# Kernel optimization log

Measured on AMD Instinct MI355X. Metric: run time of the kernel, lower is better.

The kernel has to match this reference:

```python
import jax, jax.numpy as jnp
import numpy as np

IN_F, OUT_F = 1024, 1024
NUM, K = 5, 3            # pykan defaults: num grid intervals, spline degree
X_RANGE = 1.0
LN_EPS = 1e-5
BATCH = 4096


def _make_grid():
    # pykan: linspace over [-R, R] with num+1 points, extended by k points of
    # uniform spacing h on each side -> (in_dim, num + 2k + 1)
    g = np.linspace(-X_RANGE, X_RANGE, NUM + 1)
    h = (g[-1] - g[0]) / NUM
    ext = np.concatenate([g[0] - h * np.arange(K, 0, -1), g, g[-1] + h * np.arange(1, K + 1)])
    grid = np.broadcast_to(ext, (IN_F, NUM + 2 * K + 1)).copy()
    return jnp.asarray(grid, dtype=jnp.float32)


def setup_inputs() -> dict:
    key = jax.random.key(0)
    ks = jax.random.split(key, 4)
    x = jax.random.uniform(ks[0], (BATCH, IN_F), jnp.float32, -1.0, 1.0)
    coef = jax.random.normal(ks[1], (IN_F, OUT_F, NUM + K), jnp.float32) * 0.1
    scale_base = jax.random.normal(ks[2], (IN_F, OUT_F), jnp.float32) / jnp.sqrt(jnp.float32(IN_F))
    scale_sp = jnp.ones((IN_F, OUT_F), jnp.float32)
    gamma = jnp.ones((OUT_F,), jnp.float32)   # LayerNorm weight
    beta = jnp.zeros((OUT_F,), jnp.float32)   # LayerNorm bias
    return {"x": x, "coef": coef, "scale_base": scale_base, "scale_sp": scale_sp,
            "gamma": gamma, "beta": beta, "grid": _make_grid()}


def _b_splines(x, grid, k):
    # Cox-de Boor recursion, exactly as pykan B_batch (uniform grid -> no NaNs).
    # x: (B, in), grid: (in, G) -> basis (B, in, NUM + k)
    xe = x[:, :, None]
    g = grid[None, :, :]
    B = ((xe >= g[:, :, :-1]) & (xe < g[:, :, 1:])).astype(x.dtype)
    for p in range(1, k + 1):
        B = ((xe - g[:, :, :-(p + 1)]) / (g[:, :, p:-1] - g[:, :, :-(p + 1)]) * B[:, :, :-1]
             + (g[:, :, p + 1:] - xe) / (g[:, :, p + 1:] - g[:, :, 1:-p]) * B[:, :, 1:])
    return B


def reference(x, coef, scale_base, scale_sp, gamma, beta, grid):
    basis = _b_splines(x, grid, K)                        # (B, in, NUM+K)
    spline = jnp.einsum('bik,iok->bio', basis, coef)      # (B, in, out)
    base = jax.nn.silu(x)                                 # (B, in)  pykan base_fun
    y = scale_base[None, :, :] * base[:, :, None] + scale_sp[None, :, :] * spline
    y = jnp.sum(y, axis=1)                                # (B, out)
    # LayerNorm(out_features)
    mu = jnp.mean(y, axis=-1, keepdims=True)
    var = jnp.var(y, axis=-1, keepdims=True)
    return (y - mu) * jax.lax.rsqrt(var + LN_EPS) * gamma + beta
```

## Files before the change

### kernel.cpp

```cpp
#include <hip/hip_runtime.h>

#define IN_F   1024
#define OUT_F  1024
#define BATCHN 4096
#define KDIM   9216

using i32x4 = __attribute__((ext_vector_type(4))) int;

__device__ __forceinline__ unsigned short f2bf(float f) {
  union { float f; unsigned int u; } v; v.f = f;
  unsigned int u = v.u;
  unsigned int r = (u + 0x7FFFu + ((u >> 16) & 1u)) >> 16;
  return (unsigned short)r;
}

__device__ __forceinline__ float bf2f(unsigned short h) {
  union { unsigned int u; float f; } v; v.u = ((unsigned int)h) << 16;
  return v.f;
}

#define ASCALE 172.0f

__device__ __forceinline__ unsigned char qa(float v) {
  return (unsigned char)(char)__float2int_rn(v * ASCALE);
}

__device__ __forceinline__ void async_load16(const void* g, void* l) {
  __builtin_amdgcn_global_load_lds(
      (__attribute__((address_space(1))) void*)(g),
      (__attribute__((address_space(3))) void*)(l),
      16, 0, 0);
}

__global__ __launch_bounds__(256) void kan_prep_a(const float* __restrict__ x,
                                                  const float* __restrict__ grid,
                                                  unsigned char* __restrict__ A) {
  int idx4 = blockIdx.x * 256 + threadIdx.x;
  int b  = idx4 >> 8;
  int i0 = (idx4 & 255) * 4;

  const float4 xv4 = *(const float4*)(x + (size_t)b * IN_F + i0);
  const float4* gp = (const float4*)grid;
  float4 g0 = gp[0], g1 = gp[1], g2 = gp[2];
  float t[12] = {g0.x, g0.y, g0.z, g0.w, g1.x, g1.y, g1.z, g1.w,
                 g2.x, g2.y, g2.z, g2.w};

  float inv_h = 1.0f / (t[4] - t[3]);
  const float invp[3] = {inv_h, inv_h * 0.5f, inv_h * (1.0f / 3.0f)};

  float xs[4] = {xv4.x, xv4.y, xv4.z, xv4.w};
  unsigned char o9[9][4];

#pragma unroll
  for (int e = 0; e < 4; ++e) {
    float xv = xs[e];
    float sil = xv / (1.0f + __expf(-xv));
    float B[11];
#pragma unroll
    for (int j = 0; j < 11; ++j) B[j] = (xv >= t[j] && xv < t[j + 1]) ? 1.0f : 0.0f;
#pragma unroll
    for (int p = 1; p <= 3; ++p) {
      float ip = invp[p - 1];
#pragma unroll
      for (int j = 0; j + p < 11; ++j)
        B[j] = (xv - t[j]) * ip * B[j] + (t[j + p + 1] - xv) * ip * B[j + 1];
    }
    o9[0][e] = qa(sil);
#pragma unroll
    for (int k = 0; k < 8; ++k) o9[k + 1][e] = qa(B[k]);
  }

  size_t base = (size_t)b * KDIM + i0;
#pragma unroll
  for (int tp = 0; tp < 9; ++tp)
    *(unsigned int*)(A + base + (size_t)tp * 1024) = *(const unsigned int*)&o9[tp][0];
}

__global__ __launch_bounds__(256) void kan_scales(const float* __restrict__ sb,
                                                  const float* __restrict__ ssp,
                                                  const float* __restrict__ coef,
                                                  unsigned int* __restrict__ sraw) {
  int o  = (blockIdx.x & 3) * 256 + threadIdx.x;
  int ib = (blockIdx.x >> 2) * 32;
  float m = 0.f;
  for (int ii = 0; ii < 32; ++ii) {
    int io = (ib + ii) * 1024 + o;
    float s = ssp[io];
    float mm = fabsf(sb[io]);
    const float4* cp = (const float4*)(coef + (size_t)io * 8);
    float4 c0 = cp[0], c1 = cp[1];
    mm = fmaxf(mm, fmaxf(fmaxf(fabsf(s * c0.x), fabsf(s * c0.y)),
                         fmaxf(fabsf(s * c0.z), fabsf(s * c0.w))));
    mm = fmaxf(mm, fmaxf(fmaxf(fabsf(s * c1.x), fabsf(s * c1.y)),
                         fmaxf(fabsf(s * c1.z), fabsf(s * c1.w))));
    m = fmaxf(m, mm);
  }
  atomicMax(sraw + o, __float_as_uint(m));
}

__global__ __launch_bounds__(256) void kan_prep_w(const float* __restrict__ sb,
                                                  const float* __restrict__ ssp,
                                                  const float* __restrict__ coef,
                                                  const unsigned int* __restrict__ sraw,
                                                  unsigned char* __restrict__ WT) {
  __shared__ unsigned char lds[9][128][33];
  int i0 = (blockIdx.x >> 5) * 128, o0 = (blockIdx.x & 31) * 32;
  int tid = threadIdx.x;
  int oo = tid & 31;
  float qs = 127.f / __uint_as_float(sraw[o0 + oo]);
#pragma unroll
  for (int r = 0; r < 16; ++r) {
    int idx = r * 256 + tid;
    int ii = idx >> 5;
    int io = (i0 + ii) * 1024 + (o0 + oo);
    float b = sb[io], s = ssp[io];
    const float4* cp = (const float4*)(coef + (size_t)io * 8);
    float4 c0 = cp[0], c1 = cp[1];
    lds[0][ii][oo] = (unsigned char)(char)__float2int_rn(b * qs);
    lds[1][ii][oo] = (unsigned char)(char)__float2int_rn(s * c0.x * qs);
    lds[2][ii][oo] = (unsigned char)(char)__float2int_rn(s * c0.y * qs);
    lds[3][ii][oo] = (unsigned char)(char)__float2int_rn(s * c0.z * qs);
    lds[4][ii][oo] = (unsigned char)(char)__float2int_rn(s * c0.w * qs);
    lds[5][ii][oo] = (unsigned char)(char)__float2int_rn(s * c1.x * qs);
    lds[6][ii][oo] = (unsigned char)(char)__float2int_rn(s * c1.y * qs);
    lds[7][ii][oo] = (unsigned char)(char)__float2int_rn(s * c1.z * qs);
    lds[8][ii][oo] = (unsigned char)(char)__float2int_rn(s * c1.w * qs);
  }
  __syncthreads();
  int woo = tid >> 3, ig = tid & 7;
  size_t rowbase = (size_t)(o0 + woo) * KDIM + i0 + ig * 16;
#pragma unroll
  for (int tp = 0; tp < 9; ++tp) {
    unsigned char tmp[16];
#pragma unroll
    for (int q = 0; q < 16; ++q) tmp[q] = lds[tp][ig * 16 + q][woo];
    *(uint4*)(WT + rowbase + (size_t)tp * 1024) = *(const uint4*)tmp;
  }
}

#define BM 256
#define BN 256
#define BKB 128
#define KQ     (KDIM / 4)
#define NSLI   (KQ / BKB)
#define SLOT   32768

__global__ __launch_bounds__(512, 2) void kan_gemm(const unsigned char* __restrict__ A,
                                                   const unsigned char* __restrict__ BT,
                                                   const unsigned int* __restrict__ sraw,
                                                   float* __restrict__ C,
                                                   unsigned short* __restrict__ P) {
  extern __shared__ unsigned char lds[];
  unsigned char* As = lds;
  unsigned char* Bs = lds + 3 * SLOT;
  const int tid = threadIdx.x;
  const int wid = tid >> 6, lane = tid & 63;
  const int wr = wid >> 2, wc = wid & 3;
  const int row16 = lane & 15, kgrp = lane >> 4;
  const int rswB = (row16 & 7) << 4;

  int wg = ((blockIdx.x & 7) << 5) | (blockIdx.x >> 3);
  const int s = wg >> 6;
  const int m0 = ((wg >> 2) & 15) * BM, n0 = (wg & 3) * BN;
  const size_t kbase = (size_t)s * KQ;
  const unsigned char* Ab = A;
  const unsigned char* Bb = BT;

  i32x4 acc[8][4] = {};

  auto stage = [&](const unsigned char* Gb, int grow0, unsigned char* slotp, int sl) {
    size_t kbyte = kbase + (size_t)sl * BKB;
#pragma unroll
    for (int q = 0; q < 4; ++q) {
      int d = q * 8192 + tid * 16;
      int row = d >> 7;
      int csw = (d & 127) ^ ((row & 7) << 4);
      async_load16(Gb + (size_t)(grow0 + row) * KDIM + kbyte + csw,
                   slotp + (q * 8192 + wid * 1024));
    }
  };

  stage(Ab, m0, As, 0);
  stage(Bb, n0, Bs, 0);
  stage(Ab, m0, As + SLOT, 1);

  int consA = 0;
  for (int sl = 0; sl < NSLI; ++sl) {
    if (sl < NSLI - 1) asm volatile("s_waitcnt vmcnt(4)" ::: "memory");
    else               asm volatile("s_waitcnt vmcnt(0)" ::: "memory");
    __builtin_amdgcn_s_barrier();
    __builtin_amdgcn_sched_barrier(0);
    const unsigned char* as = As + consA * SLOT;
    const unsigned char* bs = Bs + (sl & 1) * SLOT;
    const int cb0 = (kgrp << 4) ^ rswB;
    const int cb1 = (64 | (kgrp << 4)) ^ rswB;

    i32x4 b0[4], a0[4];
#pragma unroll
    for (int n = 0; n < 4; ++n)
      b0[n] = *(const i32x4*)(bs + (wc * 64 + n * 16 + row16) * 128 + cb0);
#pragma unroll
    for (int m = 0; m < 4; ++m)
      a0[m] = *(const i32x4*)(as + (wr * 128 + m * 16 + row16) * 128 + cb0);
    if (sl + 1 < NSLI) stage(Bb, n0, Bs + ((sl + 1) & 1) * SLOT, sl + 1);
    __builtin_amdgcn_sched_barrier(0);
    __builtin_amdgcn_s_barrier();
    __builtin_amdgcn_s_setprio(1);
#pragma unroll
    for (int m = 0; m < 4; ++m)
#pragma unroll
      for (int n = 0; n < 4; ++n)
        acc[m][n] = __builtin_amdgcn_mfma_i32_16x16x64_i8(a0[m], b0[n], acc[m][n], 0, 0, 0);
    __builtin_amdgcn_s_setprio(0);

    i32x4 a1[4];
#pragma unroll
    for (int m = 0; m < 4; ++m)
      a1[m] = *(const i32x4*)(as + (wr * 128 + (m + 4) * 16 + row16) * 128 + cb0);
    {
      int stgA = consA - 1; if (stgA < 0) stgA += 3;
      if (sl + 2 < NSLI) stage(Ab, m0, As + stgA * SLOT, sl + 2);
    }
    __builtin_amdgcn_sched_barrier(0);
    __builtin_amdgcn_s_barrier();
    __builtin_amdgcn_s_setprio(1);
#pragma unroll
    for (int m = 0; m < 4; ++m)
#pragma unroll
      for (int n = 0; n < 4; ++n)
        acc[m + 4][n] = __builtin_amdgcn_mfma_i32_16x16x64_i8(a1[m], b0[n], acc[m + 4][n], 0, 0, 0);
    __builtin_amdgcn_s_setprio(0);

    i32x4 b1[4], a2[4];
#pragma unroll
    for (int n = 0; n < 4; ++n)
      b1[n] = *(const i32x4*)(bs + (wc * 64 + n * 16 + row16) * 128 + cb1);
#pragma unroll
    for (int m = 0; m < 4; ++m)
      a2[m] = *(const i32x4*)(as + (wr * 128 + m * 16 + row16) * 128 + cb1);
    __builtin_amdgcn_sched_barrier(0);
    __builtin_amdgcn_s_barrier();
    __builtin_amdgcn_s_setprio(1);
#pragma unroll
    for (int m = 0; m < 4; ++m)
#pragma unroll
      for (int n = 0; n < 4; ++n)
        acc[m][n] = __builtin_amdgcn_mfma_i32_16x16x64_i8(a2[m], b1[n], acc[m][n], 0, 0, 0);
    __builtin_amdgcn_s_setprio(0);

    i32x4 a3[4];
#pragma unroll
    for (int m = 0; m < 4; ++m)
      a3[m] = *(const i32x4*)(as + (wr * 128 + (m + 4) * 16 + row16) * 128 + cb1);
    __builtin_amdgcn_sched_barrier(0);
    __builtin_amdgcn_s_barrier();
    __builtin_amdgcn_s_setprio(1);
#pragma unroll
    for (int m = 0; m < 4; ++m)
#pragma unroll
      for (int n = 0; n < 4; ++n)
        acc[m + 4][n] = __builtin_amdgcn_mfma_i32_16x16x64_i8(a3[m], b1[n], acc[m + 4][n], 0, 0, 0);
    __builtin_amdgcn_s_setprio(0);

    consA = (consA == 2) ? 0 : consA + 1;
  }

  float dq[4];
#pragma unroll
  for (int n = 0; n < 4; ++n)
    dq[n] = __uint_as_float(sraw[n0 + wc * 64 + n * 16 + row16]) * (1.f / (ASCALE * 127.f));

  if (s == 3) {
    float* Cb = C + (size_t)(m0 + wr * 128) * OUT_F + n0 + wc * 64;
#pragma unroll
    for (int m = 0; m < 8; ++m)
#pragma unroll
      for (int n = 0; n < 4; ++n)
#pragma unroll
        for (int r = 0; r < 4; ++r)
          Cb[(size_t)(m * 16 + kgrp * 4 + r) * OUT_F + n * 16 + row16] =
              (float)acc[m][n][r] * dq[n];
  } else {
    unsigned short* Pb = P + (size_t)s * BATCHN * OUT_F
                       + (size_t)(m0 + wr * 128) * OUT_F + n0 + wc * 64;
#pragma unroll
    for (int m = 0; m < 8; ++m)
#pragma unroll
      for (int n = 0; n < 4; ++n)
#pragma unroll
        for (int r = 0; r < 4; ++r)
          Pb[(size_t)(m * 16 + kgrp * 4 + r) * OUT_F + n * 16 + row16] =
              f2bf((float)acc[m][n][r] * dq[n]);
  }
}

__global__ __launch_bounds__(256) void kan_ln(float* __restrict__ y,
                                              const unsigned short* __restrict__ P,
                                              const float* __restrict__ gamma,
                                              const float* __restrict__ beta) {
  __shared__ float ss[4], ssq[4];
  int tid = threadIdx.x;
  float4* p = (float4*)(y + (size_t)blockIdx.x * OUT_F);
  float4 v = p[tid];
#pragma unroll
  for (int pp = 0; pp < 3; ++pp) {
    const ushort4 pv = ((const ushort4*)(P + (size_t)pp * BATCHN * OUT_F
                                           + (size_t)blockIdx.x * OUT_F))[tid];
    v.x += bf2f(pv.x);
    v.y += bf2f(pv.y);
    v.z += bf2f(pv.z);
    v.w += bf2f(pv.w);
  }
  float s = v.x + v.y + v.z + v.w;
  float q = v.x * v.x + v.y * v.y + v.z * v.z + v.w * v.w;
#pragma unroll
  for (int off = 1; off < 64; off <<= 1) {
    s += __shfl_xor(s, off);
    q += __shfl_xor(q, off);
  }
  if ((tid & 63) == 0) { ss[tid >> 6] = s; ssq[tid >> 6] = q; }
  __syncthreads();
  float S = ss[0] + ss[1] + ss[2] + ss[3];
  float Q = ssq[0] + ssq[1] + ssq[2] + ssq[3];
  float mu  = S * (1.0f / OUT_F);
  float var = Q * (1.0f / OUT_F) - mu * mu;
  float inv = rsqrtf(var + 1e-5f);
  const float4 g  = ((const float4*)gamma)[tid];
  const float4 bt = ((const float4*)beta)[tid];
  float4 o;
  o.x = (v.x - mu) * inv * g.x + bt.x;
  o.y = (v.y - mu) * inv * g.y + bt.y;
  o.z = (v.z - mu) * inv * g.z + bt.z;
  o.w = (v.w - mu) * inv * g.w + bt.w;
  p[tid] = o;
}

extern "C" void kernel_launch(void* const* d_in, const int* in_sizes, int n_in,
                              void* d_out, int out_size, void* d_ws, size_t ws_size,
                              hipStream_t stream) {
  const float* x     = (const float*)d_in[0];
  const float* coef  = (const float*)d_in[1];
  const float* sb    = (const float*)d_in[2];
  const float* ssp   = (const float*)d_in[3];
  const float* gamma = (const float*)d_in[4];
  const float* beta  = (const float*)d_in[5];
  const float* grid  = (const float*)d_in[6];

  const size_t a_bytes  = (size_t)BATCHN * KDIM;
  const size_t wt_bytes = (size_t)OUT_F * KDIM;
  const size_t sr_bytes = 4096;
  const size_t p_bytes  = (size_t)3 * BATCHN * OUT_F * 2;
  if (ws_size < a_bytes + wt_bytes + sr_bytes + p_bytes) return;

  unsigned char* A    = (unsigned char*)d_ws;
  unsigned char* WT   = A + a_bytes;
  unsigned int*  sraw = (unsigned int*)(WT + wt_bytes);
  unsigned short* P   = (unsigned short*)((unsigned char*)sraw + sr_bytes);
  float* y = (float*)d_out;

  const size_t lds_bytes = 5 * (size_t)SLOT;
  static bool attr_set = false;
  if (!attr_set) {
    hipFuncSetAttribute((const void*)kan_gemm,
                        hipFuncAttributeMaxDynamicSharedMemorySize, (int)lds_bytes);
    attr_set = true;
  }

  hipMemsetAsync(sraw, 0, sr_bytes, stream);
  kan_prep_a<<<dim3((BATCHN * IN_F) / 1024), dim3(256), 0, stream>>>(x, grid, A);
  kan_scales<<<dim3(128), dim3(256), 0, stream>>>(sb, ssp, coef, sraw);
  kan_prep_w<<<dim3((IN_F / 128) * (OUT_F / 32)), dim3(256), 0, stream>>>(sb, ssp, coef, sraw, WT);
  kan_gemm<<<dim3(256), dim3(512), lds_bytes, stream>>>(A, WT, sraw, y, P);
  kan_ln<<<dim3(BATCHN), dim3(256), 0, stream>>>(y, P, gamma, beta);
}
```

Baseline: 100.1 us.

## Double split-K to 8 slices with 64-byte K tiles and merge prep kernels

```diff
diff --git a/kernel.cpp b/kernel.cpp
--- a/kernel.cpp
+++ b/kernel.cpp
@@ -32,70 +32,69 @@
       16, 0, 0);
 }
 
-__global__ __launch_bounds__(256) void kan_prep_a(const float* __restrict__ x,
-                                                  const float* __restrict__ grid,
-                                                  unsigned char* __restrict__ A) {
-  int idx4 = blockIdx.x * 256 + threadIdx.x;
-  int b  = idx4 >> 8;
-  int i0 = (idx4 & 255) * 4;
-
-  const float4 xv4 = *(const float4*)(x + (size_t)b * IN_F + i0);
-  const float4* gp = (const float4*)grid;
-  float4 g0 = gp[0], g1 = gp[1], g2 = gp[2];
-  float t[12] = {g0.x, g0.y, g0.z, g0.w, g1.x, g1.y, g1.z, g1.w,
-                 g2.x, g2.y, g2.z, g2.w};
-
-  float inv_h = 1.0f / (t[4] - t[3]);
-  const float invp[3] = {inv_h, inv_h * 0.5f, inv_h * (1.0f / 3.0f)};
-
-  float xs[4] = {xv4.x, xv4.y, xv4.z, xv4.w};
-  unsigned char o9[9][4];
-
-#pragma unroll
-  for (int e = 0; e < 4; ++e) {
-    float xv = xs[e];
-    float sil = xv / (1.0f + __expf(-xv));
-    float B[11];
-#pragma unroll
-    for (int j = 0; j < 11; ++j) B[j] = (xv >= t[j] && xv < t[j + 1]) ? 1.0f : 0.0f;
-#pragma unroll
-    for (int p = 1; p <= 3; ++p) {
-      float ip = invp[p - 1];
-#pragma unroll
-      for (int j = 0; j + p < 11; ++j)
-        B[j] = (xv - t[j]) * ip * B[j] + (t[j + p + 1] - xv) * ip * B[j + 1];
+__global__ __launch_bounds__(256) void kan_prep(const float* __restrict__ x,
+                                                const float* __restrict__ grid,
+                                                const float* __restrict__ sb,
+                                                const float* __restrict__ ssp,
+                                                const float* __restrict__ coef,
+                                                unsigned char* __restrict__ A,
+                                                unsigned int* __restrict__ sraw) {
+  int bid = blockIdx.x;
+  int tid = threadIdx.x;
+  if (bid < 4096) {
+    int idx4 = bid * 256 + tid;
+    int b  = idx4 >> 8;
+    int i0 = (idx4 & 255) * 4;
+    const float4 xv4 = *(const float4*)(x + (size_t)b * IN_F + i0);
+    const float4* gp = (const float4*)grid;
+    float4 g0 = gp[0], g1 = gp[1], g2 = gp[2];
+    float t[12] = {g0.x, g0.y, g0.z, g0.w, g1.x, g1.y, g1.z, g1.w,
+                   g2.x, g2.y, g2.z, g2.w};
+    float inv_h = 1.0f / (t[4] - t[3]);
+    const float invp[3] = {inv_h, inv_h * 0.5f, inv_h * (1.0f / 3.0f)};
+    float xs[4] = {xv4.x, xv4.y, xv4.z, xv4.w};
+    unsigned char o9[9][4];
+#pragma unroll
+    for (int e = 0; e < 4; ++e) {
+      float xv = xs[e];
+      float sil = xv / (1.0f + __expf(-xv));
+      float B[11];
+#pragma unroll
+      for (int j = 0; j < 11; ++j) B[j] = (xv >= t[j] && xv < t[j + 1]) ? 1.0f : 0.0f;
+#pragma unroll
+      for (int p = 1; p <= 3; ++p) {
+        float ip = invp[p - 1];
+#pragma unroll
+        for (int j = 0; j + p < 11; ++j)
+          B[j] = (xv - t[j]) * ip * B[j] + (t[j + p + 1] - xv) * ip * B[j + 1];
+      }
+      o9[0][e] = qa(sil);
+#pragma unroll
+      for (int k = 0; k < 8; ++k) o9[k + 1][e] = qa(B[k]);
     }
-    o9[0][e] = qa(sil);
-#pragma unroll
-    for (int k = 0; k < 8; ++k) o9[k + 1][e] = qa(B[k]);
-  }
-
-  size_t base = (size_t)b * KDIM + i0;
-#pragma unroll
-  for (int tp = 0; tp < 9; ++tp)
-    *(unsigned int*)(A + base + (size_t)tp * 1024) = *(const unsigned int*)&o9[tp][0];
-}
-
-__global__ __launch_bounds__(256) void kan_scales(const float* __restrict__ sb,
-                                                  const float* __restrict__ ssp,
-                                                  const float* __restrict__ coef,
-                                                  unsigned int* __restrict__ sraw) {
-  int o  = (blockIdx.x & 3) * 256 + threadIdx.x;
-  int ib = (blockIdx.x >> 2) * 32;
-  float m = 0.f;
-  for (int ii = 0; ii < 32; ++ii) {
-    int io = (ib + ii) * 1024 + o;
-    float s = ssp[io];
-    float mm = fabsf(sb[io]);
-    const float4* cp = (const float4*)(coef + (size_t)io * 8);
-    float4 c0 = cp[0], c1 = cp[1];
-    mm = fmaxf(mm, fmaxf(fmaxf(fabsf(s * c0.x), fabsf(s * c0.y)),
-                         fmaxf(fabsf(s * c0.z), fabsf(s * c0.w))));
-    mm = fmaxf(mm, fmaxf(fmaxf(fabsf(s * c1.x), fabsf(s * c1.y)),
-                         fmaxf(fabsf(s * c1.z), fabsf(s * c1.w))));
-    m = fmaxf(m, mm);
-  }
-  atomicMax(sraw + o, __float_as_uint(m));
+    size_t base = (size_t)b * KDIM + i0;
+#pragma unroll
+    for (int tp = 0; tp < 9; ++tp)
+      *(unsigned int*)(A + base + (size_t)tp * 1024) = *(const unsigned int*)&o9[tp][0];
+  } else {
+    int b2 = bid - 4096;
+    int o  = (b2 & 3) * 256 + tid;
+    int ib = (b2 >> 2) * 32;
+    float m = 0.f;
+    for (int ii = 0; ii < 32; ++ii) {
+      int io = (ib + ii) * 1024 + o;
+      float s = ssp[io];
+      float mm = fabsf(sb[io]);
+      const float4* cp = (const float4*)(coef + (size_t)io * 8);
+      float4 c0 = cp[0], c1 = cp[1];
+      mm = fmaxf(mm, fmaxf(fmaxf(fabsf(s * c0.x), fabsf(s * c0.y)),
+                           fmaxf(fabsf(s * c0.z), fabsf(s * c0.w))));
+      mm = fmaxf(mm, fmaxf(fmaxf(fabsf(s * c1.x), fabsf(s * c1.y)),
+                           fmaxf(fabsf(s * c1.z), fabsf(s * c1.w))));
+      m = fmaxf(m, mm);
+    }
+    atomicMax(sraw + o, __float_as_uint(m));
+  }
 }
 
 __global__ __launch_bounds__(256) void kan_prep_w(const float* __restrict__ sb,
@@ -140,10 +139,11 @@
 
 #define BM 256
 #define BN 256
-#define BKB 128
-#define KQ     (KDIM / 4)
-#define NSLI   (KQ / BKB)
-#define SLOT   32768
+#define BKB 64
+#define NSP 8
+#define KQ   (KDIM / NSP)
+#define NSLI (KQ / BKB)
+#define SLOT 16384
 
 __global__ __launch_bounds__(512, 2) void kan_gemm(const unsigned char* __restrict__ A,
                                                    const unsigned char* __restrict__ BT,
@@ -157,9 +157,8 @@
   const int wid = tid >> 6, lane = tid & 63;
   const int wr = wid >> 2, wc = wid & 3;
   const int row16 = lane & 15, kgrp = lane >> 4;
-  const int rswB = (row16 & 7) << 4;
-
-  int wg = ((blockIdx.x & 7) << 5) | (blockIdx.x >> 3);
+
+  int wg = ((blockIdx.x & 7) << 6) | (blockIdx.x >> 3);
   const int s = wg >> 6;
   const int m0 = ((wg >> 2) & 15) * BM, n0 = (wg & 3) * BN;
   const size_t kbase = (size_t)s * KQ;
@@ -171,14 +170,18 @@
   auto stage = [&](const unsigned char* Gb, int grow0, unsigned char* slotp, int sl) {
     size_t kbyte = kbase + (size_t)sl * BKB;
 #pragma unroll
-    for (int q = 0; q < 4; ++q) {
+    for (int q = 0; q < 2; ++q) {
       int d = q * 8192 + tid * 16;
-      int row = d >> 7;
-      int csw = (d & 127) ^ ((row & 7) << 4);
+      int row = d >> 6;
+      int u = (d >> 4) & 3;
+      int csw = (u ^ ((row ^ (row >> 2)) & 3)) << 4;
       async_load16(Gb + (size_t)(grow0 + row) * KDIM + kbyte + csw,
                    slotp + (q * 8192 + wid * 1024));
     }
   };
+  auto raddr = [&](int row) {
+    return row * 64 + ((kgrp ^ ((row ^ (row >> 2)) & 3)) << 4);
+  };
 
   stage(Ab, m0, As, 0);
   stage(Bb, n0, Bs, 0);
@@ -186,22 +189,20 @@
 
   int consA = 0;
   for (int sl = 0; sl < NSLI; ++sl) {
-    if (sl < NSLI - 1) asm volatile("s_waitcnt vmcnt(4)" ::: "memory");
+    if (sl < NSLI - 1) asm volatile("s_waitcnt vmcnt(2)" ::: "memory");
     else               asm volatile("s_waitcnt vmcnt(0)" ::: "memory");
     __builtin_amdgcn_s_barrier();
     __builtin_amdgcn_sched_barrier(0);
     const unsigned char* as = As + consA * SLOT;
     const unsigned char* bs = Bs + (sl & 1) * SLOT;
-    const int cb0 = (kgrp << 4) ^ rswB;
-    const int cb1 = (64 | (kgrp << 4)) ^ rswB;
 
     i32x4 b0[4], a0[4];
 #pragma unroll
     for (int n = 0; n < 4; ++n)
-      b0[n] = *(const i32x4*)(bs + (wc * 64 + n * 16 + row16) * 128 + cb0);
+      b0[n] = *(const i32x4*)(bs + raddr(wc * 64 + n * 16 + row16));
 #pragma unroll
     for (int m = 0; m < 4; ++m)
-      a0[m] = *(const i32x4*)(as + (wr * 128 + m * 16 + row16) * 128 + cb0);
+      a0[m] = *(const i32x4*)(as + raddr(wr * 128 + m * 16 + row16));
     if (sl + 1 < NSLI) stage(Bb, n0, Bs + ((sl + 1) & 1) * SLOT, sl + 1);
     __builtin_amdgcn_sched_barrier(0);
     __builtin_amdgcn_s_barrier();
@@ -216,7 +217,7 @@
     i32x4 a1[4];
 #pragma unroll
     for (int m = 0; m < 4; ++m)
-      a1[m] = *(const i32x4*)(as + (wr * 128 + (m + 4) * 16 + row16) * 128 + cb0);
+      a1[m] = *(const i32x4*)(as + raddr(wr * 128 + (m + 4) * 16 + row16));
     {
       int stgA = consA - 1; if (stgA < 0) stgA += 3;
       if (sl + 2 < NSLI) stage(Ab, m0, As + stgA * SLOT, sl + 2);
@@ -231,37 +232,6 @@
         acc[m + 4][n] = __builtin_amdgcn_mfma_i32_16x16x64_i8(a1[m], b0[n], acc[m + 4][n], 0, 0, 0);
     __builtin_amdgcn_s_setprio(0);
 
-    i32x4 b1[4], a2[4];
-#pragma unroll
-    for (int n = 0; n < 4; ++n)
-      b1[n] = *(const i32x4*)(bs + (wc * 64 + n * 16 + row16) * 128 + cb1);
-#pragma unroll
-    for (int m = 0; m < 4; ++m)
-      a2[m] = *(const i32x4*)(as + (wr * 128 + m * 16 + row16) * 128 + cb1);
-    __builtin_amdgcn_sched_barrier(0);
-    __builtin_amdgcn_s_barrier();
-    __builtin_amdgcn_s_setprio(1);
-#pragma unroll
-    for (int m = 0; m < 4; ++m)
-#pragma unroll
-      for (int n = 0; n < 4; ++n)
-        acc[m][n] = __builtin_amdgcn_mfma_i32_16x16x64_i8(a2[m], b1[n], acc[m][n], 0, 0, 0);
-    __builtin_amdgcn_s_setprio(0);
-
-    i32x4 a3[4];
-#pragma unroll
-    for (int m = 0; m < 4; ++m)
-      a3[m] = *(const i32x4*)(as + (wr * 128 + (m + 4) * 16 + row16) * 128 + cb1);
-    __builtin_amdgcn_sched_barrier(0);
-    __builtin_amdgcn_s_barrier();
-    __builtin_amdgcn_s_setprio(1);
-#pragma unroll
-    for (int m = 0; m < 4; ++m)
-#pragma unroll
-      for (int n = 0; n < 4; ++n)
-        acc[m + 4][n] = __builtin_amdgcn_mfma_i32_16x16x64_i8(a3[m], b1[n], acc[m + 4][n], 0, 0, 0);
-    __builtin_amdgcn_s_setprio(0);
-
     consA = (consA == 2) ? 0 : consA + 1;
   }
 
@@ -270,7 +240,7 @@
   for (int n = 0; n < 4; ++n)
     dq[n] = __uint_as_float(sraw[n0 + wc * 64 + n * 16 + row16]) * (1.f / (ASCALE * 127.f));
 
-  if (s == 3) {
+  if (s == NSP - 1) {
     float* Cb = C + (size_t)(m0 + wr * 128) * OUT_F + n0 + wc * 64;
 #pragma unroll
     for (int m = 0; m < 8; ++m)
@@ -303,7 +273,7 @@
   float4* p = (float4*)(y + (size_t)blockIdx.x * OUT_F);
   float4 v = p[tid];
 #pragma unroll
-  for (int pp = 0; pp < 3; ++pp) {
+  for (int pp = 0; pp < NSP - 1; ++pp) {
     const ushort4 pv = ((const ushort4*)(P + (size_t)pp * BATCHN * OUT_F
                                            + (size_t)blockIdx.x * OUT_F))[tid];
     v.x += bf2f(pv.x);
@@ -349,7 +319,7 @@
   const size_t a_bytes  = (size_t)BATCHN * KDIM;
   const size_t wt_bytes = (size_t)OUT_F * KDIM;
   const size_t sr_bytes = 4096;
-  const size_t p_bytes  = (size_t)3 * BATCHN * OUT_F * 2;
+  const size_t p_bytes  = (size_t)(NSP - 1) * BATCHN * OUT_F * 2;
   if (ws_size < a_bytes + wt_bytes + sr_bytes + p_bytes) return;
 
   unsigned char* A    = (unsigned char*)d_ws;
@@ -367,9 +337,8 @@
   }
 
   hipMemsetAsync(sraw, 0, sr_bytes, stream);
-  kan_prep_a<<<dim3((BATCHN * IN_F) / 1024), dim3(256), 0, stream>>>(x, grid, A);
-  kan_scales<<<dim3(128), dim3(256), 0, stream>>>(sb, ssp, coef, sraw);
+  kan_prep<<<dim3(4096 + 128), dim3(256), 0, stream>>>(x, grid, sb, ssp, coef, A, sraw);
   kan_prep_w<<<dim3((IN_F / 128) * (OUT_F / 32)), dim3(256), 0, stream>>>(sb, ssp, coef, sraw, WT);
-  kan_gemm<<<dim3(256), dim3(512), lds_bytes, stream>>>(A, WT, sraw, y, P);
+  kan_gemm<<<dim3(NSP * (BATCHN / BM) * (OUT_F / BN)), dim3(512), lds_bytes, stream>>>(A, WT, sraw, y, P);
   kan_ln<<<dim3(BATCHN), dim3(256), 0, stream>>>(y, P, gamma, beta);
 }
```

Result: slower. 114.2 us (+14.1%).

## Merge prep_a and scales kernels; write all split-K partials as bf16

Applied to the files above, without the earlier changes.

```diff
diff --git a/kernel.cpp b/kernel.cpp
--- a/kernel.cpp
+++ b/kernel.cpp
@@ -32,70 +32,69 @@
       16, 0, 0);
 }
 
-__global__ __launch_bounds__(256) void kan_prep_a(const float* __restrict__ x,
-                                                  const float* __restrict__ grid,
-                                                  unsigned char* __restrict__ A) {
-  int idx4 = blockIdx.x * 256 + threadIdx.x;
-  int b  = idx4 >> 8;
-  int i0 = (idx4 & 255) * 4;
-
-  const float4 xv4 = *(const float4*)(x + (size_t)b * IN_F + i0);
-  const float4* gp = (const float4*)grid;
-  float4 g0 = gp[0], g1 = gp[1], g2 = gp[2];
-  float t[12] = {g0.x, g0.y, g0.z, g0.w, g1.x, g1.y, g1.z, g1.w,
-                 g2.x, g2.y, g2.z, g2.w};
-
-  float inv_h = 1.0f / (t[4] - t[3]);
-  const float invp[3] = {inv_h, inv_h * 0.5f, inv_h * (1.0f / 3.0f)};
-
-  float xs[4] = {xv4.x, xv4.y, xv4.z, xv4.w};
-  unsigned char o9[9][4];
-
-#pragma unroll
-  for (int e = 0; e < 4; ++e) {
-    float xv = xs[e];
-    float sil = xv / (1.0f + __expf(-xv));
-    float B[11];
-#pragma unroll
-    for (int j = 0; j < 11; ++j) B[j] = (xv >= t[j] && xv < t[j + 1]) ? 1.0f : 0.0f;
-#pragma unroll
-    for (int p = 1; p <= 3; ++p) {
-      float ip = invp[p - 1];
-#pragma unroll
-      for (int j = 0; j + p < 11; ++j)
-        B[j] = (xv - t[j]) * ip * B[j] + (t[j + p + 1] - xv) * ip * B[j + 1];
+__global__ __launch_bounds__(256) void kan_prep(const float* __restrict__ x,
+                                                const float* __restrict__ grid,
+                                                const float* __restrict__ sb,
+                                                const float* __restrict__ ssp,
+                                                const float* __restrict__ coef,
+                                                unsigned char* __restrict__ A,
+                                                unsigned int* __restrict__ sraw) {
+  int bid = blockIdx.x;
+  int tid = threadIdx.x;
+  if (bid < 4096) {
+    int idx4 = bid * 256 + tid;
+    int b  = idx4 >> 8;
+    int i0 = (idx4 & 255) * 4;
+    const float4 xv4 = *(const float4*)(x + (size_t)b * IN_F + i0);
+    const float4* gp = (const float4*)grid;
+    float4 g0 = gp[0], g1 = gp[1], g2 = gp[2];
+    float t[12] = {g0.x, g0.y, g0.z, g0.w, g1.x, g1.y, g1.z, g1.w,
+                   g2.x, g2.y, g2.z, g2.w};
+    float inv_h = 1.0f / (t[4] - t[3]);
+    const float invp[3] = {inv_h, inv_h * 0.5f, inv_h * (1.0f / 3.0f)};
+    float xs[4] = {xv4.x, xv4.y, xv4.z, xv4.w};
+    unsigned char o9[9][4];
+#pragma unroll
+    for (int e = 0; e < 4; ++e) {
+      float xv = xs[e];
+      float sil = xv / (1.0f + __expf(-xv));
+      float B[11];
+#pragma unroll
+      for (int j = 0; j < 11; ++j) B[j] = (xv >= t[j] && xv < t[j + 1]) ? 1.0f : 0.0f;
+#pragma unroll
+      for (int p = 1; p <= 3; ++p) {
+        float ip = invp[p - 1];
+#pragma unroll
+        for (int j = 0; j + p < 11; ++j)
+          B[j] = (xv - t[j]) * ip * B[j] + (t[j + p + 1] - xv) * ip * B[j + 1];
+      }
+      o9[0][e] = qa(sil);
+#pragma unroll
+      for (int k = 0; k < 8; ++k) o9[k + 1][e] = qa(B[k]);
     }
-    o9[0][e] = qa(sil);
-#pragma unroll
-    for (int k = 0; k < 8; ++k) o9[k + 1][e] = qa(B[k]);
-  }
-
-  size_t base = (size_t)b * KDIM + i0;
-#pragma unroll
-  for (int tp = 0; tp < 9; ++tp)
-    *(unsigned int*)(A + base + (size_t)tp * 1024) = *(const unsigned int*)&o9[tp][0];
-}
-
-__global__ __launch_bounds__(256) void kan_scales(const float* __restrict__ sb,
-                                                  const float* __restrict__ ssp,
-                                                  const float* __restrict__ coef,
-                                                  unsigned int* __restrict__ sraw) {
-  int o  = (blockIdx.x & 3) * 256 + threadIdx.x;
-  int ib = (blockIdx.x >> 2) * 32;
-  float m = 0.f;
-  for (int ii = 0; ii < 32; ++ii) {
-    int io = (ib + ii) * 1024 + o;
-    float s = ssp[io];
-    float mm = fabsf(sb[io]);
-    const float4* cp = (const float4*)(coef + (size_t)io * 8);
-    float4 c0 = cp[0], c1 = cp[1];
-    mm = fmaxf(mm, fmaxf(fmaxf(fabsf(s * c0.x), fabsf(s * c0.y)),
-                         fmaxf(fabsf(s * c0.z), fabsf(s * c0.w))));
-    mm = fmaxf(mm, fmaxf(fmaxf(fabsf(s * c1.x), fabsf(s * c1.y)),
-                         fmaxf(fabsf(s * c1.z), fabsf(s * c1.w))));
-    m = fmaxf(m, mm);
-  }
-  atomicMax(sraw + o, __float_as_uint(m));
+    size_t base = (size_t)b * KDIM + i0;
+#pragma unroll
+    for (int tp = 0; tp < 9; ++tp)
+      *(unsigned int*)(A + base + (size_t)tp * 1024) = *(const unsigned int*)&o9[tp][0];
+  } else {
+    int b2 = bid - 4096;
+    int o  = (b2 & 3) * 256 + tid;
+    int ib = (b2 >> 2) * 32;
+    float m = 0.f;
+    for (int ii = 0; ii < 32; ++ii) {
+      int io = (ib + ii) * 1024 + o;
+      float s = ssp[io];
+      float mm = fabsf(sb[io]);
+      const float4* cp = (const float4*)(coef + (size_t)io * 8);
+      float4 c0 = cp[0], c1 = cp[1];
+      mm = fmaxf(mm, fmaxf(fmaxf(fabsf(s * c0.x), fabsf(s * c0.y)),
+                           fmaxf(fabsf(s * c0.z), fabsf(s * c0.w))));
+      mm = fmaxf(mm, fmaxf(fmaxf(fabsf(s * c1.x), fabsf(s * c1.y)),
+                           fmaxf(fabsf(s * c1.z), fabsf(s * c1.w))));
+      m = fmaxf(m, mm);
+    }
+    atomicMax(sraw + o, __float_as_uint(m));
+  }
 }
 
 __global__ __launch_bounds__(256) void kan_prep_w(const float* __restrict__ sb,
@@ -141,14 +140,14 @@
 #define BM 256
 #define BN 256
 #define BKB 128
-#define KQ     (KDIM / 4)
-#define NSLI   (KQ / BKB)
-#define SLOT   32768
+#define NSP 4
+#define KQ   (KDIM / NSP)
+#define NSLI (KQ / BKB)
+#define SLOT 32768
 
 __global__ __launch_bounds__(512, 2) void kan_gemm(const unsigned char* __restrict__ A,
                                                    const unsigned char* __restrict__ BT,
                                                    const unsigned int* __restrict__ sraw,
-                                                   float* __restrict__ C,
                                                    unsigned short* __restrict__ P) {
   extern __shared__ unsigned char lds[];
   unsigned char* As = lds;
@@ -270,28 +269,16 @@
   for (int n = 0; n < 4; ++n)
     dq[n] = __uint_as_float(sraw[n0 + wc * 64 + n * 16 + row16]) * (1.f / (ASCALE * 127.f));
 
-  if (s == 3) {
-    float* Cb = C + (size_t)(m0 + wr * 128) * OUT_F + n0 + wc * 64;
-#pragma unroll
-    for (int m = 0; m < 8; ++m)
-#pragma unroll
-      for (int n = 0; n < 4; ++n)
-#pragma unroll
-        for (int r = 0; r < 4; ++r)
-          Cb[(size_t)(m * 16 + kgrp * 4 + r) * OUT_F + n * 16 + row16] =
-              (float)acc[m][n][r] * dq[n];
-  } else {
-    unsigned short* Pb = P + (size_t)s * BATCHN * OUT_F
-                       + (size_t)(m0 + wr * 128) * OUT_F + n0 + wc * 64;
-#pragma unroll
-    for (int m = 0; m < 8; ++m)
-#pragma unroll
-      for (int n = 0; n < 4; ++n)
-#pragma unroll
-        for (int r = 0; r < 4; ++r)
-          Pb[(size_t)(m * 16 + kgrp * 4 + r) * OUT_F + n * 16 + row16] =
-              f2bf((float)acc[m][n][r] * dq[n]);
-  }
+  unsigned short* Pb = P + (size_t)s * BATCHN * OUT_F
+                     + (size_t)(m0 + wr * 128) * OUT_F + n0 + wc * 64;
+#pragma unroll
+  for (int m = 0; m < 8; ++m)
+#pragma unroll
+    for (int n = 0; n < 4; ++n)
+#pragma unroll
+      for (int r = 0; r < 4; ++r)
+        Pb[(size_t)(m * 16 + kgrp * 4 + r) * OUT_F + n * 16 + row16] =
+            f2bf((float)acc[m][n][r] * dq[n]);
 }
 
 __global__ __launch_bounds__(256) void kan_ln(float* __restrict__ y,
@@ -300,10 +287,9 @@
                                               const float* __restrict__ beta) {
   __shared__ float ss[4], ssq[4];
   int tid = threadIdx.x;
-  float4* p = (float4*)(y + (size_t)blockIdx.x * OUT_F);
-  float4 v = p[tid];
-#pragma unroll
-  for (int pp = 0; pp < 3; ++pp) {
+  float4 v = {0.f, 0.f, 0.f, 0.f};
+#pragma unroll
+  for (int pp = 0; pp < NSP; ++pp) {
     const ushort4 pv = ((const ushort4*)(P + (size_t)pp * BATCHN * OUT_F
                                            + (size_t)blockIdx.x * OUT_F))[tid];
     v.x += bf2f(pv.x);
@@ -332,7 +318,7 @@
   o.y = (v.y - mu) * inv * g.y + bt.y;
   o.z = (v.z - mu) * inv * g.z + bt.z;
   o.w = (v.w - mu) * inv * g.w + bt.w;
-  p[tid] = o;
+  ((float4*)(y + (size_t)blockIdx.x * OUT_F))[tid] = o;
 }
 
 extern "C" void kernel_launch(void* const* d_in, const int* in_sizes, int n_in,
@@ -349,7 +335,7 @@
   const size_t a_bytes  = (size_t)BATCHN * KDIM;
   const size_t wt_bytes = (size_t)OUT_F * KDIM;
   const size_t sr_bytes = 4096;
-  const size_t p_bytes  = (size_t)3 * BATCHN * OUT_F * 2;
+  const size_t p_bytes  = (size_t)NSP * BATCHN * OUT_F * 2;
   if (ws_size < a_bytes + wt_bytes + sr_bytes + p_bytes) return;
 
   unsigned char* A    = (unsigned char*)d_ws;
@@ -367,9 +353,8 @@
   }
 
   hipMemsetAsync(sraw, 0, sr_bytes, stream);
-  kan_prep_a<<<dim3((BATCHN * IN_F) / 1024), dim3(256), 0, stream>>>(x, grid, A);
-  kan_scales<<<dim3(128), dim3(256), 0, stream>>>(sb, ssp, coef, sraw);
+  kan_prep<<<dim3(4096 + 128), dim3(256), 0, stream>>>(x, grid, sb, ssp, coef, A, sraw);
   kan_prep_w<<<dim3((IN_F / 128) * (OUT_F / 32)), dim3(256), 0, stream>>>(sb, ssp, coef, sraw, WT);
-  kan_gemm<<<dim3(256), dim3(512), lds_bytes, stream>>>(A, WT, sraw, y, P);
+  kan_gemm<<<dim3(NSP * (BATCHN / BM) * (OUT_F / BN)), dim3(512), lds_bytes, stream>>>(A, WT, sraw, P);
   kan_ln<<<dim3(BATCHN), dim3(256), 0, stream>>>(y, P, gamma, beta);
 }
```

Measured after the change: 93.50 us, median of 2. 1.07x faster.
